# Optimization experiments

Measured on AMD Instinct MI355X. Metric: run time of the kernel, lower is better.

The kernel has to match this reference:

```python
import jax, jax.numpy as jnp
import numpy as np

N, E, FIN, H, FO = 50000, 800000, 256, 8, 32


def setup_inputs() -> dict:
    key = jax.random.key(0)
    ks = jax.random.split(key, 7)
    node_features = jax.random.normal(ks[0], (N, FIN), dtype=jnp.float32)
    edge_index = jax.random.randint(ks[1], (2, E), 0, N, dtype=jnp.int32).astype(jnp.int64)
    # parameters (xavier-ish scaling)
    Wp = jax.random.normal(ks[2], (H * FO, FIN), dtype=jnp.float32) * (1.0 / np.sqrt(FIN))
    a_src = jax.random.normal(ks[3], (1, H, FO), dtype=jnp.float32) * 0.1
    a_trg = jax.random.normal(ks[4], (1, H, FO), dtype=jnp.float32) * 0.1
    Wskip = jax.random.normal(ks[5], (H * FO, FIN), dtype=jnp.float32) * (1.0 / np.sqrt(FIN))
    bias = jnp.zeros((H * FO,), dtype=jnp.float32)
    return {"node_features": node_features, "edge_index": edge_index,
            "Wp": Wp, "a_src": a_src, "a_trg": a_trg, "Wskip": Wskip, "bias": bias}


def reference(node_features, edge_index, Wp, a_src, a_trg, Wskip, bias):
    # dropout is identity at inference
    x = node_features                                   # [N, FIN]
    src, trg = edge_index[0], edge_index[1]             # [E], [E]
    proj = (x @ Wp.T).reshape(-1, H, FO)                # [N, H, FO]
    scores_src = jnp.sum(proj * a_src, axis=-1)         # [N, H]
    scores_trg = jnp.sum(proj * a_trg, axis=-1)         # [N, H]
    # lift to edges
    s = scores_src[src] + scores_trg[trg]               # [E, H]
    s = jax.nn.leaky_relu(s, negative_slope=0.2)
    # global max subtraction (matches torch code: scores.max())
    s = s - jnp.max(s)
    exp_s = jnp.exp(s)                                  # [E, H]
    denom = jax.ops.segment_sum(exp_s, trg, num_segments=N)   # [N, H]
    attn = exp_s / (denom[trg] + 1e-16)                 # [E, H]
    weighted = proj[src] * attn[:, :, None]             # [E, H, FO]
    out = jax.ops.segment_sum(weighted, trg, num_segments=N)  # [N, H, FO]
    # skip connection: FO != FIN, so use skip_proj
    out = out + (x @ Wskip.T).reshape(-1, H, FO)
    out = out.reshape(-1, H * FO) + bias                # concat heads
    return jax.nn.elu(out)
```

## Files before the change

### kernel.cpp

```cpp
#include <hip/hip_runtime.h>
#include <math.h>

#define FIN 256
#define HF  256
#define NH  8

typedef __bf16 bf16x8 __attribute__((ext_vector_type(8)));
typedef float  f32x4  __attribute__((ext_vector_type(4)));
typedef unsigned short u16x8 __attribute__((ext_vector_type(8)));

__device__ __forceinline__ unsigned short f2bf(float f) {
    unsigned u = __float_as_uint(f);
    unsigned r = (u + 0x7fffu + ((u >> 16) & 1u)) >> 16;
    return (unsigned short)r;
}
__device__ __forceinline__ float bf2f(unsigned short h) {
    return __uint_as_float(((unsigned)h) << 16);
}

__global__ __launch_bounds__(256) void convert_hist_k(
    const float* __restrict__ x, const float* __restrict__ Wp,
    const float* __restrict__ Wskip, unsigned short* __restrict__ A2,
    unsigned short* __restrict__ W2, const int* __restrict__ ei,
    int* __restrict__ deg, int M, int E, int convBlocks)
{
    if ((int)blockIdx.x >= convBlocks) {
        const int b = blockIdx.x - convBlocks;
        int gid = b * 256 + threadIdx.x;
        int stride = 1024 * 256;
        for (int e = gid; e < E; e += stride)
            atomicAdd(&deg[ei[(size_t)E + e]], 1);
        return;
    }
    const int l = threadIdx.x & 63;
    const int row = blockIdx.x * 4 + (threadIdx.x >> 6);
    const int total = M + 512;
    if (row >= total) return;
    const float* src;
    unsigned short* dst;
    if (row < M) { src = x + (size_t)row * 256; dst = A2 + (size_t)row * 512; }
    else {
        int j = row - M;
        src = (j < 256) ? Wp + (size_t)j * 256 : Wskip + (size_t)(j - 256) * 256;
        dst = W2 + (size_t)j * 512;
    }
    float4 v = *(const float4*)&src[l * 4];
    ushort4 h, lo;
    h.x = f2bf(v.x); lo.x = f2bf(v.x - bf2f(h.x));
    h.y = f2bf(v.y); lo.y = f2bf(v.y - bf2f(h.y));
    h.z = f2bf(v.z); lo.z = f2bf(v.z - bf2f(h.z));
    h.w = f2bf(v.w); lo.w = f2bf(v.w - bf2f(h.w));
    *(ushort4*)&dst[l * 4]       = h;
    *(ushort4*)&dst[256 + l * 4] = lo;
}

__device__ __forceinline__ void gload16(const void* g, void* l) {
    __builtin_amdgcn_global_load_lds(
        (const __attribute__((address_space(1))) void*)g,
        (__attribute__((address_space(3))) void*)l, 16, 0, 0);
}

__global__ __launch_bounds__(256) void mfma_gemm(
    const unsigned short* __restrict__ A2, const unsigned short* __restrict__ W2,
    const float* __restrict__ bias, const float* __restrict__ a_src,
    const float* __restrict__ a_trg, unsigned short* __restrict__ projb,
    float* __restrict__ ssrc, float* __restrict__ strg,
    float* __restrict__ out, int M)
{
    __shared__ __align__(16) unsigned short sAh[8192], sAl[8192], sBh[8192], sBl[8192];

    const int tid = threadIdx.x;
    const int l   = tid & 63;
    const int w   = tid >> 6;
    const int wr  = w >> 1, wc = w & 1;
    const int brow = blockIdx.x * 128;
    const int bcol = blockIdx.y * 128;

    f32x4 acc[4][4];
    #pragma unroll
    for (int a = 0; a < 4; ++a)
        #pragma unroll
        for (int b = 0; b < 4; ++b) acc[a][b] = (f32x4){0.f, 0.f, 0.f, 0.f};

    const int srow = l >> 3;
    const int sseg = (l & 7) ^ srow;

    for (int kk = 0; kk < 4; ++kk) {
        #pragma unroll
        for (int i = 0; i < 4; ++i) {
            const int rl  = w * 32 + i * 8 + srow;
            const int lds = (w * 32 + i * 8) * 64;
            int ga = brow + rl; if (ga >= M) ga = M - 1;
            const unsigned short* gA = A2 + (size_t)ga * 512 + kk * 64 + sseg * 8;
            const unsigned short* gB = W2 + (size_t)(bcol + rl) * 512 + kk * 64 + sseg * 8;
            gload16(gA,       &sAh[lds]);
            gload16(gA + 256, &sAl[lds]);
            gload16(gB,       &sBh[lds]);
            gload16(gB + 256, &sBl[lds]);
        }
        __syncthreads();

        #pragma unroll
        for (int ks = 0; ks < 2; ++ks) {
            const int sg = ((ks * 4) + (l >> 4)) ^ (l & 7);
            bf16x8 ah[4], al[4], bh[4], bl[4];
            #pragma unroll
            for (int f = 0; f < 4; ++f) {
                const int ra = wr * 64 + f * 16 + (l & 15);
                const int rb = wc * 64 + f * 16 + (l & 15);
                ah[f] = *(const bf16x8*)&sAh[ra * 64 + sg * 8];
                al[f] = *(const bf16x8*)&sAl[ra * 64 + sg * 8];
                bh[f] = *(const bf16x8*)&sBh[rb * 64 + sg * 8];
                bl[f] = *(const bf16x8*)&sBl[rb * 64 + sg * 8];
            }
            #pragma unroll
            for (int fm = 0; fm < 4; ++fm)
                #pragma unroll
                for (int fn = 0; fn < 4; ++fn) {
                    acc[fm][fn] = __builtin_amdgcn_mfma_f32_16x16x32_bf16(ah[fm], bh[fn], acc[fm][fn], 0, 0, 0);
                    acc[fm][fn] = __builtin_amdgcn_mfma_f32_16x16x32_bf16(ah[fm], bl[fn], acc[fm][fn], 0, 0, 0);
                    acc[fm][fn] = __builtin_amdgcn_mfma_f32_16x16x32_bf16(al[fm], bh[fn], acc[fm][fn], 0, 0, 0);
                }
        }
        __syncthreads();
    }

    if (bcol < 256) {
        float as[4], at[4];
        #pragma unroll
        for (int fn = 0; fn < 4; ++fn) {
            const int col = bcol + wc * 64 + fn * 16 + (l & 15);
            as[fn] = a_src[col];
            at[fn] = a_trg[col];
        }
        #pragma unroll
        for (int fn = 0; fn < 4; ++fn) {
            const int col = bcol + wc * 64 + fn * 16 + (l & 15);
            #pragma unroll
            for (int fm = 0; fm < 4; ++fm) {
                const int r0 = brow + wr * 64 + fm * 16 + (l >> 4) * 4;
                #pragma unroll
                for (int q = 0; q < 4; ++q) {
                    const int row = r0 + q;
                    if (row < M) projb[(size_t)row * 256 + col] = f2bf(acc[fm][fn][q]);
                }
            }
        }
        const int headA = ((bcol + wc * 64) >> 5);
        const int headB = headA + 1;
        #pragma unroll
        for (int fm = 0; fm < 4; ++fm) {
            #pragma unroll
            for (int q = 0; q < 4; ++q) {
                float p0 = acc[fm][0][q] * as[0] + acc[fm][1][q] * as[1];
                float p1 = acc[fm][2][q] * as[2] + acc[fm][3][q] * as[3];
                float t0 = acc[fm][0][q] * at[0] + acc[fm][1][q] * at[1];
                float t1 = acc[fm][2][q] * at[2] + acc[fm][3][q] * at[3];
                #pragma unroll
                for (int m = 1; m < 16; m <<= 1) {
                    p0 += __shfl_xor(p0, m, 64);
                    p1 += __shfl_xor(p1, m, 64);
                    t0 += __shfl_xor(t0, m, 64);
                    t1 += __shfl_xor(t1, m, 64);
                }
                if ((l & 15) == 0) {
                    const int row = brow + wr * 64 + fm * 16 + (l >> 4) * 4 + q;
                    if (row < M) {
                        ssrc[(size_t)row * NH + headA] = p0;
                        ssrc[(size_t)row * NH + headB] = p1;
                        strg[(size_t)row * NH + headA] = t0;
                        strg[(size_t)row * NH + headB] = t1;
                    }
                }
            }
        }
    } else {
        #pragma unroll
        for (int fn = 0; fn < 4; ++fn) {
            const int col = bcol + wc * 64 + fn * 16 + (l & 15);
            const float bv = bias[col - 256];
            float* dst = out + (col - 256);
            #pragma unroll
            for (int fm = 0; fm < 4; ++fm) {
                const int r0 = brow + wr * 64 + fm * 16 + (l >> 4) * 4;
                #pragma unroll
                for (int q = 0; q < 4; ++q) {
                    const int row = r0 + q;
                    if (row < M) dst[(size_t)row * 256] = acc[fm][fn][q] + bv;
                }
            }
        }
    }
}

__device__ __forceinline__ float lrelu(float v) { return v > 0.f ? v : 0.2f * v; }

__global__ __launch_bounds__(256) void scan1_k(
    const int* __restrict__ deg, int* __restrict__ rp, int* __restrict__ bsum, int N)
{
    __shared__ int sh[256];
    const int tid = threadIdx.x;
    const int base = blockIdx.x * 4096 + tid * 16;
    int v[16], pre[16];
    int s = 0;
    #pragma unroll
    for (int i = 0; i < 16; ++i) {
        int idx = base + i;
        v[i] = (idx < N) ? deg[idx] : 0;
        pre[i] = s; s += v[i];
    }
    sh[tid] = s;
    __syncthreads();
    #pragma unroll
    for (int off = 1; off < 256; off <<= 1) {
        int t = (tid >= off) ? sh[tid - off] : 0;
        __syncthreads();
        sh[tid] += t;
        __syncthreads();
    }
    int texcl = sh[tid] - s;
    #pragma unroll
    for (int i = 0; i < 16; ++i) {
        int idx = base + i;
        if (idx < N) rp[idx] = texcl + pre[i];
    }
    if (tid == 255) bsum[blockIdx.x] = sh[255];
}

__global__ void scan2_k(int* bsum, int nsb) {
    if (threadIdx.x == 0 && blockIdx.x == 0) {
        int s = 0;
        for (int b = 0; b < nsb; ++b) { int v = bsum[b]; bsum[b] = s; s += v; }
    }
}

__global__ __launch_bounds__(256) void scan3_k(
    int* __restrict__ rp, const int* __restrict__ bsum,
    int* __restrict__ cursor, int N, int E)
{
    int gid = blockIdx.x * 256 + threadIdx.x;
    if (gid < N) {
        int v = rp[gid] + bsum[gid >> 12];
        rp[gid] = v;
        cursor[gid] = v;
    }
    if (gid == 0) rp[N] = E;
}

__global__ __launch_bounds__(256) void scatter_k(
    const int* __restrict__ ei, int* __restrict__ cursor,
    int* __restrict__ col, int E)
{
    int gid = blockIdx.x * 256 + threadIdx.x;
    int stride = gridDim.x * 256;
    for (int e = gid; e < E; e += stride) {
        int s = ei[e];
        int t = ei[(size_t)E + e];
        int pos = atomicAdd(&cursor[t], 1);
        col[pos] = s;
    }
}

__global__ __launch_bounds__(256) void gather_k(
    const int* __restrict__ rp, const int* __restrict__ col,
    const float* __restrict__ ssrc, const float* __restrict__ strg,
    const unsigned short* __restrict__ projb, float* __restrict__ out, int N)
{
    const int lane = threadIdx.x & 63;
    const int node = blockIdx.x * 4 + (threadIdx.x >> 6);
    if (node >= N) return;
    const int half = lane >> 5;
    const int hl   = lane & 31;
    const int h    = hl >> 2;

    const float st = strg[(size_t)node * NH + h];
    const int beg = rp[node], end = rp[node + 1];

    float a0 = 0.f, a1 = 0.f, a2 = 0.f, a3 = 0.f,
          a4 = 0.f, a5 = 0.f, a6 = 0.f, a7 = 0.f, den = 0.f;

    for (int i0 = beg; i0 < end; i0 += 64) {
        int ci = (i0 + lane < end) ? col[i0 + lane] : 0;
        int cnt = end - i0; if (cnt > 64) cnt = 64;
        #pragma unroll 2
        for (int k = 0; k < cnt; k += 2) {
            int s = __shfl(ci, k + half, 64);
            bool act = (k + half) < cnt;
            float es = act ? __expf(lrelu(ssrc[(size_t)s * NH + h] + st)) : 0.f;
            u16x8 r = *(const u16x8*)&projb[(size_t)s * HF + hl * 8];
            a0 += bf2f(r[0]) * es;  a1 += bf2f(r[1]) * es;
            a2 += bf2f(r[2]) * es;  a3 += bf2f(r[3]) * es;
            a4 += bf2f(r[4]) * es;  a5 += bf2f(r[5]) * es;
            a6 += bf2f(r[6]) * es;  a7 += bf2f(r[7]) * es;
            den += es;
        }
    }

    a0 += __shfl_xor(a0, 32, 64);  a1 += __shfl_xor(a1, 32, 64);
    a2 += __shfl_xor(a2, 32, 64);  a3 += __shfl_xor(a3, 32, 64);
    a4 += __shfl_xor(a4, 32, 64);  a5 += __shfl_xor(a5, 32, 64);
    a6 += __shfl_xor(a6, 32, 64);  a7 += __shfl_xor(a7, 32, 64);
    den += __shfl_xor(den, 32, 64);

    const float inv = 1.f / (den + 1e-16f);
    const size_t ob = (size_t)node * HF + hl * 8 + half * 4;
    float4 sk = *(const float4*)&out[ob];
    float c0, c1, c2, c3;
    if (half == 0) { c0 = a0; c1 = a1; c2 = a2; c3 = a3; }
    else           { c0 = a4; c1 = a5; c2 = a6; c3 = a7; }
    float4 v;
    v.x = c0 * inv + sk.x;
    v.y = c1 * inv + sk.y;
    v.z = c2 * inv + sk.z;
    v.w = c3 * inv + sk.w;
    v.x = v.x > 0.f ? v.x : expm1f(v.x);
    v.y = v.y > 0.f ? v.y : expm1f(v.y);
    v.z = v.z > 0.f ? v.z : expm1f(v.z);
    v.w = v.w > 0.f ? v.w : expm1f(v.w);
    *(float4*)&out[ob] = v;
}

extern "C" void kernel_launch(void* const* d_in, const int* in_sizes, int n_in,
                              void* d_out, int out_size, void* d_ws, size_t ws_size,
                              hipStream_t stream) {
    const float* x     = (const float*)d_in[0];
    const int*   ei    = (const int*)d_in[1];
    const float* Wp    = (const float*)d_in[2];
    const float* a_src = (const float*)d_in[3];
    const float* a_trg = (const float*)d_in[4];
    const float* Wskip = (const float*)d_in[5];
    const float* bias  = (const float*)d_in[6];
    float* out = (float*)d_out;

    const int N = in_sizes[0] / FIN;
    const int E = in_sizes[1] / 2;
    const int nsb = (N + 4095) / 4096;

    unsigned short* projb = (unsigned short*)d_ws;
    float* ssrc          = (float*)(projb + (size_t)N * HF);
    float* strg          = ssrc + (size_t)N * NH;
    unsigned short* A2   = (unsigned short*)(strg + (size_t)N * NH);
    unsigned short* W2   = A2 + (size_t)N * 512;
    int* deg             = (int*)(W2 + 512 * 512);
    int* rp              = deg + N;
    int* cursor          = rp + (N + 1);
    int* bsum            = cursor + N;
    int* col             = bsum + 16;

    hipMemsetAsync(deg, 0, (size_t)N * sizeof(int), stream);

    const int convBlocks = (N + 512 + 3) / 4;
    convert_hist_k<<<convBlocks + 1024, 256, 0, stream>>>(
        x, Wp, Wskip, A2, W2, ei, deg, N, E, convBlocks);

    dim3 ggrid((N + 127) / 128, 4);
    mfma_gemm<<<ggrid, 256, 0, stream>>>(A2, W2, bias, a_src, a_trg,
                                         projb, ssrc, strg, out, N);

    scan1_k<<<nsb, 256, 0, stream>>>(deg, rp, bsum, N);
    scan2_k<<<1, 64, 0, stream>>>(bsum, nsb);
    scan3_k<<<(N + 255) / 256, 256, 0, stream>>>(rp, bsum, cursor, N, E);

    scatter_k<<<1024, 256, 0, stream>>>(ei, cursor, col, E);

    gather_k<<<(N + 3) / 4, 256, 0, stream>>>(rp, col, ssrc, strg, projb, out, N);
}
```

Baseline: 358.9 us.

## Halve GEMM K-tile, merge scan into one block, unroll gather by two edges

The GEMM now stages 32-wide K slices (half the LDS footprint) over 8 iterations instead of 64-wide over 4. The aim is more resident blocks per CU, at the cost of twice as many barriers. The three-kernel prefix scan becomes a single 1024-thread block scan, removing two launches but serialising per-thread chunks. The gather loop now has each half-wave process two edges per step, with manual bf16 unpacking, to expose more memory-level parallelism.

```diff
diff --git a/kernel.cpp b/kernel.cpp
--- a/kernel.cpp
+++ b/kernel.cpp
@@ -7,7 +7,6 @@
 
 typedef __bf16 bf16x8 __attribute__((ext_vector_type(8)));
 typedef float  f32x4  __attribute__((ext_vector_type(4)));
-typedef unsigned short u16x8 __attribute__((ext_vector_type(8)));
 
 __device__ __forceinline__ unsigned short f2bf(float f) {
     unsigned u = __float_as_uint(f);
@@ -67,7 +66,7 @@
     float* __restrict__ ssrc, float* __restrict__ strg,
     float* __restrict__ out, int M)
 {
-    __shared__ __align__(16) unsigned short sAh[8192], sAl[8192], sBh[8192], sBl[8192];
+    __shared__ __align__(16) unsigned short sAh[4096], sAl[4096], sBh[4096], sBl[4096];
 
     const int tid = threadIdx.x;
     const int l   = tid & 63;
@@ -82,17 +81,18 @@
         #pragma unroll
         for (int b = 0; b < 4; ++b) acc[a][b] = (f32x4){0.f, 0.f, 0.f, 0.f};
 
-    const int srow = l >> 3;
-    const int sseg = (l & 7) ^ srow;
-
-    for (int kk = 0; kk < 4; ++kk) {
-        #pragma unroll
-        for (int i = 0; i < 4; ++i) {
-            const int rl  = w * 32 + i * 8 + srow;
-            const int lds = (w * 32 + i * 8) * 64;
-            int ga = brow + rl; if (ga >= M) ga = M - 1;
-            const unsigned short* gA = A2 + (size_t)ga * 512 + kk * 64 + sseg * 8;
-            const unsigned short* gB = W2 + (size_t)(bcol + rl) * 512 + kk * 64 + sseg * 8;
+    const int srow = l >> 2;
+    const int sseg = (l & 3) ^ (srow & 3);
+
+    for (int kk = 0; kk < 8; ++kk) {
+        #pragma unroll
+        for (int i = 0; i < 2; ++i) {
+            const int rl0 = w * 32 + i * 16;
+            const int lds = rl0 * 32;
+            int ga = brow + rl0 + srow; if (ga >= M) ga = M - 1;
+            const int gb = bcol + rl0 + srow;
+            const unsigned short* gA = A2 + (size_t)ga * 512 + kk * 32 + sseg * 8;
+            const unsigned short* gB = W2 + (size_t)gb * 512 + kk * 32 + sseg * 8;
             gload16(gA,       &sAh[lds]);
             gload16(gA + 256, &sAl[lds]);
             gload16(gB,       &sBh[lds]);
@@ -100,28 +100,25 @@
         }
         __syncthreads();
 
-        #pragma unroll
-        for (int ks = 0; ks < 2; ++ks) {
-            const int sg = ((ks * 4) + (l >> 4)) ^ (l & 7);
-            bf16x8 ah[4], al[4], bh[4], bl[4];
+        const int sg = (l >> 4) ^ (l & 3);
+        bf16x8 ah[4], al[4], bh[4], bl[4];
+        #pragma unroll
+        for (int f = 0; f < 4; ++f) {
+            const int ra = wr * 64 + f * 16 + (l & 15);
+            const int rb = wc * 64 + f * 16 + (l & 15);
+            ah[f] = *(const bf16x8*)&sAh[ra * 32 + sg * 8];
+            al[f] = *(const bf16x8*)&sAl[ra * 32 + sg * 8];
+            bh[f] = *(const bf16x8*)&sBh[rb * 32 + sg * 8];
+            bl[f] = *(const bf16x8*)&sBl[rb * 32 + sg * 8];
+        }
+        #pragma unroll
+        for (int fm = 0; fm < 4; ++fm)
             #pragma unroll
-            for (int f = 0; f < 4; ++f) {
-                const int ra = wr * 64 + f * 16 + (l & 15);
-                const int rb = wc * 64 + f * 16 + (l & 15);
-                ah[f] = *(const bf16x8*)&sAh[ra * 64 + sg * 8];
-                al[f] = *(const bf16x8*)&sAl[ra * 64 + sg * 8];
-                bh[f] = *(const bf16x8*)&sBh[rb * 64 + sg * 8];
-                bl[f] = *(const bf16x8*)&sBl[rb * 64 + sg * 8];
+            for (int fn = 0; fn < 4; ++fn) {
+                acc[fm][fn] = __builtin_amdgcn_mfma_f32_16x16x32_bf16(ah[fm], bh[fn], acc[fm][fn], 0, 0, 0);
+                acc[fm][fn] = __builtin_amdgcn_mfma_f32_16x16x32_bf16(ah[fm], bl[fn], acc[fm][fn], 0, 0, 0);
+                acc[fm][fn] = __builtin_amdgcn_mfma_f32_16x16x32_bf16(al[fm], bh[fn], acc[fm][fn], 0, 0, 0);
             }
-            #pragma unroll
-            for (int fm = 0; fm < 4; ++fm)
-                #pragma unroll
-                for (int fn = 0; fn < 4; ++fn) {
-                    acc[fm][fn] = __builtin_amdgcn_mfma_f32_16x16x32_bf16(ah[fm], bh[fn], acc[fm][fn], 0, 0, 0);
-                    acc[fm][fn] = __builtin_amdgcn_mfma_f32_16x16x32_bf16(ah[fm], bl[fn], acc[fm][fn], 0, 0, 0);
-                    acc[fm][fn] = __builtin_amdgcn_mfma_f32_16x16x32_bf16(al[fm], bh[fn], acc[fm][fn], 0, 0, 0);
-                }
-        }
         __syncthreads();
     }
 
@@ -195,56 +192,32 @@
 
 __device__ __forceinline__ float lrelu(float v) { return v > 0.f ? v : 0.2f * v; }
 
-__global__ __launch_bounds__(256) void scan1_k(
-    const int* __restrict__ deg, int* __restrict__ rp, int* __restrict__ bsum, int N)
-{
-    __shared__ int sh[256];
-    const int tid = threadIdx.x;
-    const int base = blockIdx.x * 4096 + tid * 16;
-    int v[16], pre[16];
+__global__ __launch_bounds__(1024) void scan_k(
+    const int* __restrict__ deg, int* __restrict__ rp,
+    int* __restrict__ cursor, int N, int E)
+{
+    __shared__ int sh[1024];
+    const int t = threadIdx.x;
+    const int C = (N + 1023) >> 10;
+    const int b0 = t * C;
+    const int b1 = min(b0 + C, N);
     int s = 0;
-    #pragma unroll
-    for (int i = 0; i < 16; ++i) {
-        int idx = base + i;
-        v[i] = (idx < N) ? deg[idx] : 0;
-        pre[i] = s; s += v[i];
-    }
-    sh[tid] = s;
+    for (int i = b0; i < b1; ++i) s += deg[i];
+    sh[t] = s;
     __syncthreads();
     #pragma unroll
-    for (int off = 1; off < 256; off <<= 1) {
-        int t = (tid >= off) ? sh[tid - off] : 0;
+    for (int off = 1; off < 1024; off <<= 1) {
+        int v = (t >= off) ? sh[t - off] : 0;
         __syncthreads();
-        sh[tid] += t;
+        sh[t] += v;
         __syncthreads();
     }
-    int texcl = sh[tid] - s;
-    #pragma unroll
-    for (int i = 0; i < 16; ++i) {
-        int idx = base + i;
-        if (idx < N) rp[idx] = texcl + pre[i];
-    }
-    if (tid == 255) bsum[blockIdx.x] = sh[255];
-}
-
-__global__ void scan2_k(int* bsum, int nsb) {
-    if (threadIdx.x == 0 && blockIdx.x == 0) {
-        int s = 0;
-        for (int b = 0; b < nsb; ++b) { int v = bsum[b]; bsum[b] = s; s += v; }
-    }
-}
-
-__global__ __launch_bounds__(256) void scan3_k(
-    int* __restrict__ rp, const int* __restrict__ bsum,
-    int* __restrict__ cursor, int N, int E)
-{
-    int gid = blockIdx.x * 256 + threadIdx.x;
-    if (gid < N) {
-        int v = rp[gid] + bsum[gid >> 12];
-        rp[gid] = v;
-        cursor[gid] = v;
-    }
-    if (gid == 0) rp[N] = E;
+    int excl = sh[t] - s;
+    for (int i = b0; i < b1; ++i) {
+        rp[i] = excl; cursor[i] = excl;
+        excl += deg[i];
+    }
+    if (t == 0) rp[N] = E;
 }
 
 __global__ __launch_bounds__(256) void scatter_k(
@@ -282,17 +255,24 @@
     for (int i0 = beg; i0 < end; i0 += 64) {
         int ci = (i0 + lane < end) ? col[i0 + lane] : 0;
         int cnt = end - i0; if (cnt > 64) cnt = 64;
-        #pragma unroll 2
-        for (int k = 0; k < cnt; k += 2) {
-            int s = __shfl(ci, k + half, 64);
-            bool act = (k + half) < cnt;
-            float es = act ? __expf(lrelu(ssrc[(size_t)s * NH + h] + st)) : 0.f;
-            u16x8 r = *(const u16x8*)&projb[(size_t)s * HF + hl * 8];
-            a0 += bf2f(r[0]) * es;  a1 += bf2f(r[1]) * es;
-            a2 += bf2f(r[2]) * es;  a3 += bf2f(r[3]) * es;
-            a4 += bf2f(r[4]) * es;  a5 += bf2f(r[5]) * es;
-            a6 += bf2f(r[6]) * es;  a7 += bf2f(r[7]) * es;
-            den += es;
+        for (int k = 0; k < cnt; k += 4) {
+            const int e0 = k + half * 2, e1 = e0 + 1;
+            int s0 = __shfl(ci, e0 < 64 ? e0 : 63, 64);
+            int s1 = __shfl(ci, e1 < 64 ? e1 : 63, 64);
+            const bool v0 = e0 < cnt, v1 = e1 < cnt;
+            uint4 r0 = *(const uint4*)&projb[(size_t)s0 * HF + hl * 8];
+            uint4 r1 = *(const uint4*)&projb[(size_t)s1 * HF + hl * 8];
+            float es0 = v0 ? __expf(lrelu(ssrc[(size_t)s0 * NH + h] + st)) : 0.f;
+            float es1 = v1 ? __expf(lrelu(ssrc[(size_t)s1 * NH + h] + st)) : 0.f;
+            a0 += __uint_as_float(r0.x << 16) * es0 + __uint_as_float(r1.x << 16) * es1;
+            a1 += __uint_as_float(r0.x & 0xffff0000u) * es0 + __uint_as_float(r1.x & 0xffff0000u) * es1;
+            a2 += __uint_as_float(r0.y << 16) * es0 + __uint_as_float(r1.y << 16) * es1;
+            a3 += __uint_as_float(r0.y & 0xffff0000u) * es0 + __uint_as_float(r1.y & 0xffff0000u) * es1;
+            a4 += __uint_as_float(r0.z << 16) * es0 + __uint_as_float(r1.z << 16) * es1;
+            a5 += __uint_as_float(r0.z & 0xffff0000u) * es0 + __uint_as_float(r1.z & 0xffff0000u) * es1;
+            a6 += __uint_as_float(r0.w << 16) * es0 + __uint_as_float(r1.w << 16) * es1;
+            a7 += __uint_as_float(r0.w & 0xffff0000u) * es0 + __uint_as_float(r1.w & 0xffff0000u) * es1;
+            den += es0 + es1;
         }
     }
 
@@ -334,7 +314,6 @@
 
     const int N = in_sizes[0] / FIN;
     const int E = in_sizes[1] / 2;
-    const int nsb = (N + 4095) / 4096;
 
     unsigned short* projb = (unsigned short*)d_ws;
     float* ssrc          = (float*)(projb + (size_t)N * HF);
@@ -344,8 +323,7 @@
     int* deg             = (int*)(W2 + 512 * 512);
     int* rp              = deg + N;
     int* cursor          = rp + (N + 1);
-    int* bsum            = cursor + N;
-    int* col             = bsum + 16;
+    int* col             = cursor + N;
 
     hipMemsetAsync(deg, 0, (size_t)N * sizeof(int), stream);
 
@@ -357,9 +335,7 @@
     mfma_gemm<<<ggrid, 256, 0, stream>>>(A2, W2, bias, a_src, a_trg,
                                          projb, ssrc, strg, out, N);
 
-    scan1_k<<<nsb, 256, 0, stream>>>(deg, rp, bsum, N);
-    scan2_k<<<1, 64, 0, stream>>>(bsum, nsb);
-    scan3_k<<<(N + 255) / 256, 256, 0, stream>>>(rp, bsum, cursor, N, E);
+    scan_k<<<1, 1024, 0, stream>>>(deg, rp, cursor, N, E);
 
     scatter_k<<<1024, 256, 0, stream>>>(ei, cursor, col, E);
 
```

New measurement: 458.5 us. 1.28x slower.
